# Kernel tuning notes

Hardware: AMD Instinct MI355X
Metric: run time of the kernel (lower is better)

Reference implementation:

```python
import jax, jax.numpy as jnp
import numpy as np

N = 50000   # num nodes
E = 600000  # num edges per signed adjacency
D = 128     # feature dim
K = 10      # num_diff_layers
C = 0.15    # restart probability


def setup_inputs() -> dict:
    key = jax.random.key(0)
    ks = jax.random.split(key, 8)
    rows_p = jax.random.randint(ks[0], (E,), 0, N, dtype=jnp.int32)
    cols_p = jax.random.randint(ks[1], (E,), 0, N, dtype=jnp.int32)
    vals_p = jax.random.uniform(ks[2], (E,), dtype=jnp.float32)
    rows_m = jax.random.randint(ks[3], (E,), 0, N, dtype=jnp.int32)
    cols_m = jax.random.randint(ks[4], (E,), 0, N, dtype=jnp.int32)
    vals_m = jax.random.uniform(ks[5], (E,), dtype=jnp.float32)
    X = jax.random.normal(ks[6], (N, D), dtype=jnp.float32)
    # torch code draws old_M ~ Uniform(-1, 1) at forward time; we expose it as input
    M0 = jax.random.uniform(ks[7], (N, D), dtype=jnp.float32, minval=-1.0, maxval=1.0)
    return {"rows_p": rows_p, "cols_p": cols_p, "vals_p": vals_p,
            "rows_m": rows_m, "cols_m": cols_m, "vals_m": vals_m,
            "X": X, "M0": M0}


def _spmm(rows, cols, vals, dense):
    # COO sparse [N,N] @ dense [N,D]: gather columns, scale, scatter-add to rows
    return jax.ops.segment_sum(vals[:, None] * dense[cols], rows,
                               num_segments=dense.shape[0])


def reference(rows_p, cols_p, vals_p, rows_m, cols_m, vals_m, X, M0):
    tilda_X = C * X  # restart term
    P, M = X, M0
    for _ in range(K):
        new_P = _spmm(rows_p, cols_p, vals_p, P) + _spmm(rows_m, cols_m, vals_m, M) + tilda_X
        new_M = _spmm(rows_m, cols_m, vals_m, P) + _spmm(rows_p, cols_p, vals_p, M)
        P, M = new_P, new_M
    return (P, M)
```

## Files before the change

kernel.cpp:

```cpp
#include <hip/hip_runtime.h>
#include <math.h>


#define TB 256

__device__ __forceinline__ unsigned pack_bf16(float a, float b) {
    unsigned ua = __float_as_uint(a), ub = __float_as_uint(b);
    ua += 0x7fffu + ((ua >> 16) & 1u);
    ub += 0x7fffu + ((ub >> 16) & 1u);
    return (ua >> 16) | (ub & 0xffff0000u);
}

__device__ __forceinline__ float2 unpack_bf16(unsigned w) {
    float2 r;
    r.x = __uint_as_float(w << 16);
    r.y = __uint_as_float(w & 0xffff0000u);
    return r;
}

__global__ void zero_int_kernel(int* __restrict__ p, int n) {
    int i = blockIdx.x * blockDim.x + threadIdx.x;
    if (i < n) p[i] = 0;
}

__global__ void hist2_kernel(const int* __restrict__ rows_p, const int* __restrict__ rows_m,
                             int E, int* __restrict__ cnt) {
    int e = blockIdx.x * blockDim.x + threadIdx.x;
    if (e < 2 * E) {
        int r = (e < E) ? rows_p[e] : rows_m[e - E];
        atomicAdd(&cnt[r], 1);
    }
}

__global__ void scanA_kernel(const int* __restrict__ cnt, int* __restrict__ bsum, int n) {
    __shared__ int wsum[16];
    int tid = threadIdx.x, lane = tid & 63, wid = tid >> 6;
    int i = blockIdx.x * 1024 + tid;
    int x = (i < n) ? cnt[i] : 0;
#pragma unroll
    for (int o = 1; o < 64; o <<= 1) { int y = __shfl_up(x, o); if (lane >= o) x += y; }
    if (lane == 63) wsum[wid] = x;
    __syncthreads();
    if (tid == 0) {
        int s = 0;
#pragma unroll
        for (int w = 0; w < 16; ++w) s += wsum[w];
        bsum[blockIdx.x] = s;
    }
}

__global__ void scanB_kernel(int* __restrict__ bsum, int nb) {
    __shared__ int wsum[16];
    int tid = threadIdx.x, lane = tid & 63, wid = tid >> 6;
    int x = (tid < nb) ? bsum[tid] : 0;
    int incl = x;
#pragma unroll
    for (int o = 1; o < 64; o <<= 1) { int y = __shfl_up(incl, o); if (lane >= o) incl += y; }
    if (lane == 63) wsum[wid] = incl;
    __syncthreads();
    if (wid == 0) {
        int s = (lane < 16) ? wsum[lane] : 0;
#pragma unroll
        for (int o = 1; o < 16; o <<= 1) { int y = __shfl_up(s, o); if (lane >= o) s += y; }
        if (lane < 16) wsum[lane] = s;
    }
    __syncthreads();
    int base = (wid > 0) ? wsum[wid - 1] : 0;
    if (tid < nb) bsum[tid] = base + incl - x;
}

__global__ void scanC_kernel(const int* __restrict__ cnt, const int* __restrict__ bsum,
                             int* __restrict__ off, int* __restrict__ cur, int n) {
    __shared__ int wsum[16];
    int tid = threadIdx.x, lane = tid & 63, wid = tid >> 6;
    int i = blockIdx.x * 1024 + tid;
    int x = (i < n) ? cnt[i] : 0;
    int incl = x;
#pragma unroll
    for (int o = 1; o < 64; o <<= 1) { int y = __shfl_up(incl, o); if (lane >= o) incl += y; }
    if (lane == 63) wsum[wid] = incl;
    __syncthreads();
    if (wid == 0) {
        int s = (lane < 16) ? wsum[lane] : 0;
#pragma unroll
        for (int o = 1; o < 16; o <<= 1) { int y = __shfl_up(s, o); if (lane >= o) s += y; }
        if (lane < 16) wsum[lane] = s;
    }
    __syncthreads();
    int base = bsum[blockIdx.x] + ((wid > 0) ? wsum[wid - 1] : 0);
    if (i < n) {
        int ex = base + incl - x;
        off[i] = ex;
        cur[i] = ex;
        if (i == n - 1) off[n] = base + incl;
    }
}

__global__ void fill2_kernel(const int* __restrict__ rows_p, const int* __restrict__ cols_p,
                             const float* __restrict__ vals_p,
                             const int* __restrict__ rows_m, const int* __restrict__ cols_m,
                             const float* __restrict__ vals_m, int E,
                             int* __restrict__ cur, int2* __restrict__ edge) {
    int e = blockIdx.x * blockDim.x + threadIdx.x;
    if (e < 2 * E) {
        int r, c; float v;
        if (e < E) { r = rows_p[e]; c = cols_p[e]; v =  vals_p[e]; }
        else       { r = rows_m[e - E]; c = cols_m[e - E]; v = -vals_m[e - E]; }
        int p = atomicAdd(&cur[r], 1);
        unsigned long long rec = (unsigned)c |
            ((unsigned long long)(unsigned)__float_as_int(v) << 32);
        __builtin_nontemporal_store(rec, (unsigned long long*)&edge[p]);
    }
}

__global__ void init_kernel(const float* __restrict__ X, const float* __restrict__ M0,
                            uint2* __restrict__ SD, uint2* __restrict__ tXb, int n32) {
    int i = blockIdx.x * blockDim.x + threadIdx.x;
    if (i < n32) {
        int r = i >> 5, q = i & 31;
        float4 x = ((const float4*)X)[(size_t)r * 32 + q];
        float4 m = ((const float4*)M0)[(size_t)r * 32 + q];
        SD[(size_t)r * 64 + q]      = make_uint2(pack_bf16(x.x + m.x, x.y + m.y),
                                                 pack_bf16(x.z + m.z, x.w + m.w));
        SD[(size_t)r * 64 + 32 + q] = make_uint2(pack_bf16(x.x - m.x, x.y - m.y),
                                                 pack_bf16(x.z - m.z, x.w - m.w));
        tXb[(size_t)r * 32 + q]     = make_uint2(pack_bf16(0.15f * x.x, 0.15f * x.y),
                                                 pack_bf16(0.15f * x.z, 0.15f * x.w));
    }
}

__global__ void final_kernel(const uint2* __restrict__ SD,
                             float* __restrict__ P, float* __restrict__ M, int n32) {
    int i = blockIdx.x * blockDim.x + threadIdx.x;
    if (i < n32) {
        int r = i >> 5, q = i & 31;
        uint2 ws = SD[(size_t)r * 64 + q];
        uint2 wd = SD[(size_t)r * 64 + 32 + q];
        float2 s0 = unpack_bf16(ws.x), s1 = unpack_bf16(ws.y);
        float2 d0 = unpack_bf16(wd.x), d1 = unpack_bf16(wd.y);
        float4 p4 = make_float4(0.5f * (s0.x + d0.x), 0.5f * (s0.y + d0.y),
                                0.5f * (s1.x + d1.x), 0.5f * (s1.y + d1.y));
        float4 m4 = make_float4(0.5f * (s0.x - d0.x), 0.5f * (s0.y - d0.y),
                                0.5f * (s1.x - d1.x), 0.5f * (s1.y - d1.y));
        ((float4*)P)[(size_t)r * 32 + q] = p4;
        ((float4*)M)[(size_t)r * 32 + q] = m4;
    }
}

__global__ __launch_bounds__(TB) void layer_kernel(
    const int* __restrict__ off, const int2* __restrict__ edge,
    const uint2* __restrict__ In, uint2* __restrict__ Out,
    const uint2* __restrict__ tXb, int N) {
    int row = blockIdx.x * 4 + (threadIdx.x >> 6);
    if (row >= N) return;
    int lane = threadIdx.x & 63;
    int sel = lane >> 5;
    int q = lane & 31;

    uint2 t = tXb[(size_t)row * 32 + q];
    float2 t0 = unpack_bf16(t.x), t1 = unpack_bf16(t.y);
    float a0 = t0.x, a1 = t0.y, a2 = t1.x, a3 = t1.y;

    int bg = off[row], e = off[row + 1];
    int j = bg;
    for (; j + 8 <= e; j += 8) {
        int2 e0 = edge[j],     e1 = edge[j + 1], e2 = edge[j + 2], e3 = edge[j + 3];
        int2 e4 = edge[j + 4], e5 = edge[j + 5], e6 = edge[j + 6], e7 = edge[j + 7];
        uint2 w0 = In[(size_t)e0.x * 64 + lane];
        uint2 w1 = In[(size_t)e1.x * 64 + lane];
        uint2 w2 = In[(size_t)e2.x * 64 + lane];
        uint2 w3 = In[(size_t)e3.x * 64 + lane];
        uint2 w4 = In[(size_t)e4.x * 64 + lane];
        uint2 w5 = In[(size_t)e5.x * 64 + lane];
        uint2 w6 = In[(size_t)e6.x * 64 + lane];
        uint2 w7 = In[(size_t)e7.x * 64 + lane];
        float v0 = __int_as_float(e0.y), v1 = __int_as_float(e1.y);
        float v2 = __int_as_float(e2.y), v3 = __int_as_float(e3.y);
        float v4 = __int_as_float(e4.y), v5 = __int_as_float(e5.y);
        float v6 = __int_as_float(e6.y), v7 = __int_as_float(e7.y);
        if (!sel) {
            v0 = fabsf(v0); v1 = fabsf(v1); v2 = fabsf(v2); v3 = fabsf(v3);
            v4 = fabsf(v4); v5 = fabsf(v5); v6 = fabsf(v6); v7 = fabsf(v7);
        }
        float2 g0a = unpack_bf16(w0.x), g0b = unpack_bf16(w0.y);
        float2 g1a = unpack_bf16(w1.x), g1b = unpack_bf16(w1.y);
        float2 g2a = unpack_bf16(w2.x), g2b = unpack_bf16(w2.y);
        float2 g3a = unpack_bf16(w3.x), g3b = unpack_bf16(w3.y);
        float2 g4a = unpack_bf16(w4.x), g4b = unpack_bf16(w4.y);
        float2 g5a = unpack_bf16(w5.x), g5b = unpack_bf16(w5.y);
        float2 g6a = unpack_bf16(w6.x), g6b = unpack_bf16(w6.y);
        float2 g7a = unpack_bf16(w7.x), g7b = unpack_bf16(w7.y);
        a0 += v0 * g0a.x + v1 * g1a.x + v2 * g2a.x + v3 * g3a.x
            + v4 * g4a.x + v5 * g5a.x + v6 * g6a.x + v7 * g7a.x;
        a1 += v0 * g0a.y + v1 * g1a.y + v2 * g2a.y + v3 * g3a.y
            + v4 * g4a.y + v5 * g5a.y + v6 * g6a.y + v7 * g7a.y;
        a2 += v0 * g0b.x + v1 * g1b.x + v2 * g2b.x + v3 * g3b.x
            + v4 * g4b.x + v5 * g5b.x + v6 * g6b.x + v7 * g7b.x;
        a3 += v0 * g0b.y + v1 * g1b.y + v2 * g2b.y + v3 * g3b.y
            + v4 * g4b.y + v5 * g5b.y + v6 * g6b.y + v7 * g7b.y;
    }
    for (; j < e; ++j) {
        int2 ed = edge[j];
        uint2 w = In[(size_t)ed.x * 64 + lane];
        float v = __int_as_float(ed.y);
        if (!sel) v = fabsf(v);
        float2 ga = unpack_bf16(w.x), gb = unpack_bf16(w.y);
        a0 += v * ga.x; a1 += v * ga.y; a2 += v * gb.x; a3 += v * gb.y;
    }
    Out[(size_t)row * 64 + lane] = make_uint2(pack_bf16(a0, a1), pack_bf16(a2, a3));
}

extern "C" void kernel_launch(void* const* d_in, const int* in_sizes, int n_in,
                              void* d_out, int out_size, void* d_ws, size_t ws_size,
                              hipStream_t stream) {
    const int*   rows_p = (const int*)d_in[0];
    const int*   cols_p = (const int*)d_in[1];
    const float* vals_p = (const float*)d_in[2];
    const int*   rows_m = (const int*)d_in[3];
    const int*   cols_m = (const int*)d_in[4];
    const float* vals_m = (const float*)d_in[5];
    const float* X      = (const float*)d_in[6];
    const float* M0     = (const float*)d_in[7];

    const int E = in_sizes[0];
    const int D = 128;
    const int N = in_sizes[6] / D;
    const int K = 10;
    const int E2 = 2 * E;
    const size_t ND = (size_t)N * D;
    const int N32 = N * 32;

    float* outP = (float*)d_out;
    float* outM = outP + ND;

    char* ws = (char*)d_ws;
    size_t o = 0;
    auto alloc = [&](size_t b) -> void* {
        void* p = ws + o;
        o += (b + 255) & ~(size_t)255;
        return p;
    };
    uint2* SDA  = (uint2*)alloc((size_t)N * 64 * 8);
    uint2* SDB  = (uint2*)alloc((size_t)N * 64 * 8);
    uint2* tXb  = (uint2*)alloc((size_t)N * 32 * 8);
    int*   cnt  = (int*)alloc((size_t)N * sizeof(int));
    int*   off  = (int*)alloc((size_t)(N + 1) * sizeof(int));
    int*   cur  = (int*)alloc((size_t)N * sizeof(int));
    int*   bsum = (int*)alloc(1024 * sizeof(int));
    int2*  edge = (int2*)alloc((size_t)E2 * sizeof(int2));

    int gN   = (N + TB - 1) / TB;
    int gE2  = (E2 + TB - 1) / TB;
    int gN32 = (N32 + TB - 1) / TB;
    int nb   = (N + 1023) / 1024;

    zero_int_kernel<<<gN, TB, 0, stream>>>(cnt, N);
    hist2_kernel<<<gE2, TB, 0, stream>>>(rows_p, rows_m, E, cnt);
    scanA_kernel<<<nb, 1024, 0, stream>>>(cnt, bsum, N);
    scanB_kernel<<<1, 1024, 0, stream>>>(bsum, nb);
    scanC_kernel<<<nb, 1024, 0, stream>>>(cnt, bsum, off, cur, N);
    fill2_kernel<<<gE2, TB, 0, stream>>>(rows_p, cols_p, vals_p,
                                         rows_m, cols_m, vals_m, E, cur, edge);

    init_kernel<<<gN32, TB, 0, stream>>>(X, M0, SDA, tXb, N32);

    int gL = (N + 3) / 4;
    uint2 *Si = SDA, *So = SDB;
    for (int k = 0; k < K; ++k) {
        layer_kernel<<<gL, TB, 0, stream>>>(off, edge, Si, So, tXb, N);
        uint2* t = Si; Si = So; So = t;
    }

    final_kernel<<<gN32, TB, 0, stream>>>(Si, outP, outM, N32);
}
```

Before: 1.093 ms.

## Build CSR via two-level bucket partition and fuse final unpack into last layer

Replaces the global per-row atomic histogram, three-pass scan and atomic scatter fill with a bucketed counting sort. Edges are first partitioned into 128 row buckets of 512 rows using shared-memory histograms, then each bucket is sorted into CSR order locally in shared memory, which cuts contended global atomics and scattered writes. The final layer also writes fp32 P and M directly through a cross-half shuffle, removing the separate final kernel and one full pass over the state. The packed key stores row and column in 16 bits each, so it only holds while N fits in 65536.

New measurement: 1.006 ms. 1.09x faster.

```diff
diff --git a/kernel.cpp b/kernel.cpp
--- a/kernel.cpp
+++ b/kernel.cpp
@@ -23,93 +23,128 @@
     if (i < n) p[i] = 0;
 }
 
-__global__ void hist2_kernel(const int* __restrict__ rows_p, const int* __restrict__ rows_m,
-                             int E, int* __restrict__ cnt) {
-    int e = blockIdx.x * blockDim.x + threadIdx.x;
-    if (e < 2 * E) {
+__global__ void bucket_count_kernel(const int* __restrict__ rows_p,
+                                    const int* __restrict__ rows_m,
+                                    int E, int* __restrict__ bcnt) {
+    __shared__ int h[128];
+    for (int i = threadIdx.x; i < 128; i += TB) h[i] = 0;
+    __syncthreads();
+    int total = 2 * E;
+    for (int e = blockIdx.x * TB + threadIdx.x; e < total; e += gridDim.x * TB) {
         int r = (e < E) ? rows_p[e] : rows_m[e - E];
-        atomicAdd(&cnt[r], 1);
-    }
-}
-
-__global__ void scanA_kernel(const int* __restrict__ cnt, int* __restrict__ bsum, int n) {
-    __shared__ int wsum[16];
-    int tid = threadIdx.x, lane = tid & 63, wid = tid >> 6;
-    int i = blockIdx.x * 1024 + tid;
-    int x = (i < n) ? cnt[i] : 0;
-#pragma unroll
-    for (int o = 1; o < 64; o <<= 1) { int y = __shfl_up(x, o); if (lane >= o) x += y; }
-    if (lane == 63) wsum[wid] = x;
-    __syncthreads();
-    if (tid == 0) {
-        int s = 0;
-#pragma unroll
-        for (int w = 0; w < 16; ++w) s += wsum[w];
-        bsum[blockIdx.x] = s;
-    }
-}
-
-__global__ void scanB_kernel(int* __restrict__ bsum, int nb) {
-    __shared__ int wsum[16];
-    int tid = threadIdx.x, lane = tid & 63, wid = tid >> 6;
-    int x = (tid < nb) ? bsum[tid] : 0;
-    int incl = x;
-#pragma unroll
-    for (int o = 1; o < 64; o <<= 1) { int y = __shfl_up(incl, o); if (lane >= o) incl += y; }
-    if (lane == 63) wsum[wid] = incl;
-    __syncthreads();
-    if (wid == 0) {
-        int s = (lane < 16) ? wsum[lane] : 0;
-#pragma unroll
-        for (int o = 1; o < 16; o <<= 1) { int y = __shfl_up(s, o); if (lane >= o) s += y; }
-        if (lane < 16) wsum[lane] = s;
-    }
-    __syncthreads();
-    int base = (wid > 0) ? wsum[wid - 1] : 0;
-    if (tid < nb) bsum[tid] = base + incl - x;
-}
-
-__global__ void scanC_kernel(const int* __restrict__ cnt, const int* __restrict__ bsum,
-                             int* __restrict__ off, int* __restrict__ cur, int n) {
-    __shared__ int wsum[16];
-    int tid = threadIdx.x, lane = tid & 63, wid = tid >> 6;
-    int i = blockIdx.x * 1024 + tid;
-    int x = (i < n) ? cnt[i] : 0;
-    int incl = x;
-#pragma unroll
-    for (int o = 1; o < 64; o <<= 1) { int y = __shfl_up(incl, o); if (lane >= o) incl += y; }
-    if (lane == 63) wsum[wid] = incl;
-    __syncthreads();
-    if (wid == 0) {
-        int s = (lane < 16) ? wsum[lane] : 0;
-#pragma unroll
-        for (int o = 1; o < 16; o <<= 1) { int y = __shfl_up(s, o); if (lane >= o) s += y; }
-        if (lane < 16) wsum[lane] = s;
-    }
-    __syncthreads();
-    int base = bsum[blockIdx.x] + ((wid > 0) ? wsum[wid - 1] : 0);
-    if (i < n) {
-        int ex = base + incl - x;
-        off[i] = ex;
-        cur[i] = ex;
-        if (i == n - 1) off[n] = base + incl;
-    }
-}
-
-__global__ void fill2_kernel(const int* __restrict__ rows_p, const int* __restrict__ cols_p,
-                             const float* __restrict__ vals_p,
-                             const int* __restrict__ rows_m, const int* __restrict__ cols_m,
-                             const float* __restrict__ vals_m, int E,
-                             int* __restrict__ cur, int2* __restrict__ edge) {
-    int e = blockIdx.x * blockDim.x + threadIdx.x;
-    if (e < 2 * E) {
-        int r, c; float v;
-        if (e < E) { r = rows_p[e]; c = cols_p[e]; v =  vals_p[e]; }
+        atomicAdd(&h[r >> 9], 1);
+    }
+    __syncthreads();
+    for (int i = threadIdx.x; i < 128; i += TB)
+        if (h[i]) atomicAdd(&bcnt[i], h[i]);
+}
+
+__global__ void bucket_scan_kernel(const int* __restrict__ bcnt,
+                                   int* __restrict__ boff, int* __restrict__ bcur) {
+    int l = threadIdx.x;
+    int v0 = bcnt[l], v1 = bcnt[l + 64];
+    int i0 = v0, i1 = v1;
+#pragma unroll
+    for (int o = 1; o < 64; o <<= 1) { int y = __shfl_up(i0, o); if (l >= o) i0 += y; }
+#pragma unroll
+    for (int o = 1; o < 64; o <<= 1) { int y = __shfl_up(i1, o); if (l >= o) i1 += y; }
+    int t0 = __shfl(i0, 63);
+    int e0 = i0 - v0;
+    int e1 = i1 - v1 + t0;
+    boff[l] = e0;      boff[l + 64] = e1;
+    bcur[l] = e0;      bcur[l + 64] = e1;
+    if (l == 63) boff[128] = i1 + t0;
+}
+
+__global__ __launch_bounds__(TB) void partition_kernel(
+    const int* __restrict__ rows_p, const int* __restrict__ cols_p,
+    const float* __restrict__ vals_p,
+    const int* __restrict__ rows_m, const int* __restrict__ cols_m,
+    const float* __restrict__ vals_m, int E,
+    int* __restrict__ bcur_g, uint2* __restrict__ stage) {
+    __shared__ unsigned keys[2048];
+    __shared__ float    vals[2048];
+    __shared__ unsigned skeys[2048];
+    __shared__ float    svals[2048];
+    __shared__ int h[128], boff[128], bcur[128], bbase[128];
+    int tile0 = blockIdx.x * 2048;
+    int cnt = min(2048, 2 * E - tile0);
+
+    for (int i = threadIdx.x; i < cnt; i += TB) {
+        int e = tile0 + i; int r, c; float v;
+        if (e < E) { r = rows_p[e]; c = cols_p[e]; v = vals_p[e]; }
         else       { r = rows_m[e - E]; c = cols_m[e - E]; v = -vals_m[e - E]; }
-        int p = atomicAdd(&cur[r], 1);
-        unsigned long long rec = (unsigned)c |
-            ((unsigned long long)(unsigned)__float_as_int(v) << 32);
-        __builtin_nontemporal_store(rec, (unsigned long long*)&edge[p]);
+        keys[i] = ((unsigned)r << 16) | (unsigned)c;
+        vals[i] = v;
+    }
+    for (int i = threadIdx.x; i < 128; i += TB) { h[i] = 0; bcur[i] = 0; }
+    __syncthreads();
+    for (int i = threadIdx.x; i < cnt; i += TB) atomicAdd(&h[keys[i] >> 25], 1);
+    __syncthreads();
+    if (threadIdx.x < 64) {
+        int l = threadIdx.x;
+        int v0 = h[l], v1 = h[l + 64], i0 = v0, i1 = v1;
+#pragma unroll
+        for (int o = 1; o < 64; o <<= 1) { int y = __shfl_up(i0, o); if (l >= o) i0 += y; }
+#pragma unroll
+        for (int o = 1; o < 64; o <<= 1) { int y = __shfl_up(i1, o); if (l >= o) i1 += y; }
+        int t0 = __shfl(i0, 63);
+        boff[l] = i0 - v0;
+        boff[l + 64] = i1 - v1 + t0;
+    }
+    __syncthreads();
+    for (int i = threadIdx.x; i < cnt; i += TB) {
+        unsigned k = keys[i]; int b = k >> 25;
+        int p = boff[b] + atomicAdd(&bcur[b], 1);
+        skeys[p] = k; svals[p] = vals[i];
+    }
+    __syncthreads();
+    if (threadIdx.x < 128) {
+        int c_ = h[threadIdx.x];
+        if (c_) bbase[threadIdx.x] = atomicAdd(&bcur_g[threadIdx.x], c_);
+    }
+    __syncthreads();
+    for (int i = threadIdx.x; i < cnt; i += TB) {
+        unsigned k = skeys[i]; int b = k >> 25;
+        stage[bbase[b] + (i - boff[b])] = make_uint2(k, __float_as_uint(svals[i]));
+    }
+}
+
+__global__ __launch_bounds__(TB) void csr_finalize_kernel(
+    const uint2* __restrict__ stage, const int* __restrict__ boff_g,
+    int NBv, int N, int E2, int* __restrict__ off, int2* __restrict__ edge) {
+    __shared__ int rc[512], ro[512], rcur[512];
+    int b = blockIdx.x;
+    int row0 = b << 9;
+    int s0 = boff_g[b], s1 = boff_g[b + 1];
+    for (int i = threadIdx.x; i < 512; i += TB) { rc[i] = 0; rcur[i] = 0; }
+    __syncthreads();
+    for (int i = s0 + threadIdx.x; i < s1; i += TB)
+        atomicAdd(&rc[(stage[i].x >> 16) - row0], 1);
+    __syncthreads();
+    if (threadIdx.x < 64) {
+        int l = threadIdx.x;
+        int s = 0, loc[8];
+#pragma unroll
+        for (int j = 0; j < 8; ++j) { loc[j] = s; s += rc[l * 8 + j]; }
+        int incl = s;
+#pragma unroll
+        for (int o = 1; o < 64; o <<= 1) { int y = __shfl_up(incl, o); if (l >= o) incl += y; }
+        int base = incl - s;
+#pragma unroll
+        for (int j = 0; j < 8; ++j) ro[l * 8 + j] = base + loc[j];
+    }
+    __syncthreads();
+    for (int i = threadIdx.x; i < 512; i += TB) {
+        int r = row0 + i;
+        if (r < N) off[r] = s0 + ro[i];
+    }
+    if (b == NBv - 1 && threadIdx.x == 0) off[N] = E2;
+    for (int i = s0 + threadIdx.x; i < s1; i += TB) {
+        uint2 rec = stage[i];
+        int lr = (int)(rec.x >> 16) - row0;
+        int p = s0 + ro[lr] + atomicAdd(&rcur[lr], 1);
+        edge[p] = make_int2((int)(rec.x & 0xffffu), (int)rec.y);
     }
 }
 
@@ -129,28 +164,11 @@
     }
 }
 
-__global__ void final_kernel(const uint2* __restrict__ SD,
-                             float* __restrict__ P, float* __restrict__ M, int n32) {
-    int i = blockIdx.x * blockDim.x + threadIdx.x;
-    if (i < n32) {
-        int r = i >> 5, q = i & 31;
-        uint2 ws = SD[(size_t)r * 64 + q];
-        uint2 wd = SD[(size_t)r * 64 + 32 + q];
-        float2 s0 = unpack_bf16(ws.x), s1 = unpack_bf16(ws.y);
-        float2 d0 = unpack_bf16(wd.x), d1 = unpack_bf16(wd.y);
-        float4 p4 = make_float4(0.5f * (s0.x + d0.x), 0.5f * (s0.y + d0.y),
-                                0.5f * (s1.x + d1.x), 0.5f * (s1.y + d1.y));
-        float4 m4 = make_float4(0.5f * (s0.x - d0.x), 0.5f * (s0.y - d0.y),
-                                0.5f * (s1.x - d1.x), 0.5f * (s1.y - d1.y));
-        ((float4*)P)[(size_t)r * 32 + q] = p4;
-        ((float4*)M)[(size_t)r * 32 + q] = m4;
-    }
-}
-
 __global__ __launch_bounds__(TB) void layer_kernel(
     const int* __restrict__ off, const int2* __restrict__ edge,
     const uint2* __restrict__ In, uint2* __restrict__ Out,
-    const uint2* __restrict__ tXb, int N) {
+    const uint2* __restrict__ tXb,
+    float* __restrict__ Pout, float* __restrict__ Mout, int last, int N) {
     int row = blockIdx.x * 4 + (threadIdx.x >> 6);
     if (row >= N) return;
     int lane = threadIdx.x & 63;
@@ -207,7 +225,22 @@
         float2 ga = unpack_bf16(w.x), gb = unpack_bf16(w.y);
         a0 += v * ga.x; a1 += v * ga.y; a2 += v * gb.x; a3 += v * gb.y;
     }
-    Out[(size_t)row * 64 + lane] = make_uint2(pack_bf16(a0, a1), pack_bf16(a2, a3));
+
+    if (!last) {
+        Out[(size_t)row * 64 + lane] = make_uint2(pack_bf16(a0, a1), pack_bf16(a2, a3));
+    } else {
+        float b0 = __shfl_xor(a0, 32), b1 = __shfl_xor(a1, 32);
+        float b2 = __shfl_xor(a2, 32), b3 = __shfl_xor(a3, 32);
+        if (sel == 0) {
+            ((float4*)Pout)[(size_t)row * 32 + q] =
+                make_float4(0.5f * (a0 + b0), 0.5f * (a1 + b1),
+                            0.5f * (a2 + b2), 0.5f * (a3 + b3));
+        } else {
+            ((float4*)Mout)[(size_t)row * 32 + q] =
+                make_float4(0.5f * (b0 - a0), 0.5f * (b1 - a1),
+                            0.5f * (b2 - a2), 0.5f * (b3 - a3));
+        }
+    }
 }
 
 extern "C" void kernel_launch(void* const* d_in, const int* in_sizes, int n_in,
@@ -229,6 +262,7 @@
     const int E2 = 2 * E;
     const size_t ND = (size_t)N * D;
     const int N32 = N * 32;
+    const int NBv = (N + 511) >> 9;
 
     float* outP = (float*)d_out;
     float* outM = outP + ND;
@@ -243,33 +277,32 @@
     uint2* SDA  = (uint2*)alloc((size_t)N * 64 * 8);
     uint2* SDB  = (uint2*)alloc((size_t)N * 64 * 8);
     uint2* tXb  = (uint2*)alloc((size_t)N * 32 * 8);
-    int*   cnt  = (int*)alloc((size_t)N * sizeof(int));
     int*   off  = (int*)alloc((size_t)(N + 1) * sizeof(int));
-    int*   cur  = (int*)alloc((size_t)N * sizeof(int));
-    int*   bsum = (int*)alloc(1024 * sizeof(int));
     int2*  edge = (int2*)alloc((size_t)E2 * sizeof(int2));
-
-    int gN   = (N + TB - 1) / TB;
-    int gE2  = (E2 + TB - 1) / TB;
+    int*   bcnt = (int*)alloc(128 * sizeof(int));
+    int*   boff = (int*)alloc(129 * sizeof(int));
+    int*   bcur = (int*)alloc(128 * sizeof(int));
+    uint2* stage = SDB;
+
     int gN32 = (N32 + TB - 1) / TB;
-    int nb   = (N + 1023) / 1024;
-
-    zero_int_kernel<<<gN, TB, 0, stream>>>(cnt, N);
-    hist2_kernel<<<gE2, TB, 0, stream>>>(rows_p, rows_m, E, cnt);
-    scanA_kernel<<<nb, 1024, 0, stream>>>(cnt, bsum, N);
-    scanB_kernel<<<1, 1024, 0, stream>>>(bsum, nb);
-    scanC_kernel<<<nb, 1024, 0, stream>>>(cnt, bsum, off, cur, N);
-    fill2_kernel<<<gE2, TB, 0, stream>>>(rows_p, cols_p, vals_p,
-                                         rows_m, cols_m, vals_m, E, cur, edge);
+    int gTiles = (E2 + 2047) / 2048;
+
+    zero_int_kernel<<<1, 128, 0, stream>>>(bcnt, 128);
+    bucket_count_kernel<<<512, TB, 0, stream>>>(rows_p, rows_m, E, bcnt);
+    bucket_scan_kernel<<<1, 64, 0, stream>>>(bcnt, boff, bcur);
+    partition_kernel<<<gTiles, TB, 0, stream>>>(rows_p, cols_p, vals_p,
+                                                rows_m, cols_m, vals_m, E,
+                                                bcur, stage);
+    csr_finalize_kernel<<<NBv, TB, 0, stream>>>(stage, boff, NBv, N, E2, off, edge);
 
     init_kernel<<<gN32, TB, 0, stream>>>(X, M0, SDA, tXb, N32);
 
     int gL = (N + 3) / 4;
     uint2 *Si = SDA, *So = SDB;
     for (int k = 0; k < K; ++k) {
-        layer_kernel<<<gL, TB, 0, stream>>>(off, edge, Si, So, tXb, N);
+        int last = (k == K - 1);
+        layer_kernel<<<gL, TB, 0, stream>>>(off, edge, Si, So, tXb,
+                                            outP, outM, last, N);
         uint2* t = Si; Si = So; So = t;
     }
-
-    final_kernel<<<gN32, TB, 0, stream>>>(Si, outP, outM, N32);
-}
+}
```
